# Kernel optimization log

Hardware: AMD Instinct MI355X
Metric: run time of the kernel (lower is better)

The kernel has to match this reference:

```python
import jax, jax.numpy as jnp
import numpy as np

B, NP, K = 8, 512, 64   # graphs, points per graph, knn neighbors
N = B * NP              # total nodes
EPS = 1e-5


def knn_edges(pos):
    """knn_graph(pos, k=K, batch, loop=True): edges (src=j neighbor, dst=i)."""
    p = pos.reshape(B, NP, 3)
    d2 = jnp.sum((p[:, :, None, :] - p[:, None, :, :]) ** 2, axis=-1)  # [B,NP,NP]
    _, idx = jax.lax.top_k(-d2, K)  # [B,NP,K] nearest (self included, d2=0)
    off = (jnp.arange(B, dtype=jnp.int32) * NP)[:, None, None]
    src = (idx.astype(jnp.int32) + off).reshape(-1)
    dst = jnp.broadcast_to(jnp.arange(NP, dtype=jnp.int32)[None, :, None] + off,
                           (B, NP, K)).reshape(-1)
    return src, dst


def graph_norm(x, batch, w, b, ms):
    """PyG GraphNorm: per-graph mean/std with learnable mean scale."""
    cnt = jax.ops.segment_sum(jnp.ones((x.shape[0], 1), x.dtype), batch, B)
    mean = jax.ops.segment_sum(x, batch, B) / cnt
    out = x - mean[batch] * ms
    var = jax.ops.segment_sum(out * out, batch, B) / cnt
    return w * out / jnp.sqrt(var + EPS)[batch] + b


def pointnet_layer(h, pos, src, dst, w1, b1, w2, b2):
    """message = MLP(concat(h_j, pos_j - pos_i)); aggregate = scatter-max over dst."""
    m = jnp.concatenate([h[src], pos[src] - pos[dst]], axis=-1)  # [E, Cin+3]
    m = jax.nn.relu(m @ w1 + b1) @ w2 + b2                        # [E, Cout]
    return jax.ops.segment_max(m, dst, N)


def _forward(batch, pos,
             gn1_w, gn1_b, gn1_ms, gn2_w, gn2_b, gn2_ms, gn3_w, gn3_b, gn3_ms,
             gn4_w, gn4_b, gn4_ms, gn5_w, gn5_b, gn5_ms, gn6_w, gn6_b, gn6_ms,
             c1_w1, c1_b1, c1_w2, c1_b2, c2_w1, c2_b1, c2_w2, c2_b2,
             c3_w1, c3_b1, c3_w2, c3_b2, c4_w1, c4_b1, c4_w2, c4_b2,
             c5_w1, c5_b1, c5_w2, c5_b2, cls_w, cls_b):
    src, dst = knn_edges(pos)
    h = graph_norm(pos, batch, gn1_w, gn1_b, gn1_ms)
    h = pointnet_layer(h, pos, src, dst, c1_w1, c1_b1, c1_w2, c1_b2)
    h = jax.nn.relu(graph_norm(h, batch, gn2_w, gn2_b, gn2_ms))
    h = pointnet_layer(h, pos, src, dst, c2_w1, c2_b1, c2_w2, c2_b2)
    h = jax.nn.relu(graph_norm(h, batch, gn3_w, gn3_b, gn3_ms))
    h = pointnet_layer(h, pos, src, dst, c3_w1, c3_b1, c3_w2, c3_b2)
    h = jax.nn.relu(graph_norm(h, batch, gn4_w, gn4_b, gn4_ms))
    h = pointnet_layer(h, pos, src, dst, c4_w1, c4_b1, c4_w2, c4_b2)
    h = jax.nn.relu(graph_norm(h, batch, gn5_w, gn5_b, gn5_ms))
    h = pointnet_layer(h, pos, src, dst, c5_w1, c5_b1, c5_w2, c5_b2)
    h = jax.nn.relu(graph_norm(h, batch, gn6_w, gn6_b, gn6_ms))
    return h @ cls_w + cls_b  # [N, 14]


def setup_inputs() -> dict:
    key = jax.random.key(0)
    ks = iter(jax.random.split(key, 40))
    inp = {}
    inp["pos"] = jax.random.normal(next(ks), (N, 3), jnp.float32)
    inp["batch"] = jnp.repeat(jnp.arange(B, dtype=jnp.int32), NP)
    for i, c in enumerate([3, 64, 128, 256, 512, 512], 1):
        inp[f"gn{i}_w"] = jnp.ones((c,), jnp.float32)
        inp[f"gn{i}_b"] = jnp.zeros((c,), jnp.float32)
        inp[f"gn{i}_ms"] = jnp.ones((c,), jnp.float32)
    for i, (ci, co) in enumerate([(3, 64), (64, 128), (128, 256), (256, 512), (512, 512)], 1):
        fin = ci + 3
        inp[f"c{i}_w1"] = jax.random.normal(next(ks), (fin, co), jnp.float32) / np.sqrt(fin).astype(np.float32)
        inp[f"c{i}_b1"] = jnp.zeros((co,), jnp.float32)
        inp[f"c{i}_w2"] = jax.random.normal(next(ks), (co, co), jnp.float32) / np.sqrt(co).astype(np.float32)
        inp[f"c{i}_b2"] = jnp.zeros((co,), jnp.float32)
    inp["cls_w"] = jax.random.normal(next(ks), (512, 14), jnp.float32) / np.float32(np.sqrt(512))
    inp["cls_b"] = jnp.zeros((14,), jnp.float32)
    return inp


def reference(pos, batch,
              gn1_w, gn1_b, gn1_ms, gn2_w, gn2_b, gn2_ms, gn3_w, gn3_b, gn3_ms,
              gn4_w, gn4_b, gn4_ms, gn5_w, gn5_b, gn5_ms, gn6_w, gn6_b, gn6_ms,
              c1_w1, c1_b1, c1_w2, c1_b2, c2_w1, c2_b1, c2_w2, c2_b2,
              c3_w1, c3_b1, c3_w2, c3_b2, c4_w1, c4_b1, c4_w2, c4_b2,
              c5_w1, c5_b1, c5_w2, c5_b2, cls_w, cls_b):
    return _forward(batch, pos,
                    gn1_w, gn1_b, gn1_ms, gn2_w, gn2_b, gn2_ms, gn3_w, gn3_b, gn3_ms,
                    gn4_w, gn4_b, gn4_ms, gn5_w, gn5_b, gn5_ms, gn6_w, gn6_b, gn6_ms,
                    c1_w1, c1_b1, c1_w2, c1_b2, c2_w1, c2_b1, c2_w2, c2_b2,
                    c3_w1, c3_b1, c3_w2, c3_b2, c4_w1, c4_b1, c4_w2, c4_b2,
                    c5_w1, c5_b1, c5_w2, c5_b2, cls_w, cls_b)
```

## Files before the change

kernel.cpp:

```cpp
#include <hip/hip_runtime.h>
#include <stdint.h>

#define N_NODES 4096
#define NGRAPH 8
#define NPTS 512
#define KNN 64
#define EPSN 1e-5f

typedef _Float16 f16x8 __attribute__((ext_vector_type(8)));
typedef float f32x4 __attribute__((ext_vector_type(4)));
typedef unsigned long long u64;

__device__ __forceinline__ unsigned short f2h(float f) {
    _Float16 h = (_Float16)f;
    union { _Float16 h; unsigned short u; } cv; cv.h = h;
    return cv.u;
}

__device__ __forceinline__ void w2cv(const float* __restrict__ src, unsigned short* __restrict__ dst,
                                     int off, int lg2c) {
    int C = 1 << lg2c;
    int k = off >> lg2c, n = off & (C - 1);
    int d = ((n >> 4) * (C / 32) + (k >> 5)) * 512 + ((k >> 3) & 3) * 128 + (n & 15) * 8 + (k & 7);
    dst[d] = f2h(src[off]);
}

__global__ __launch_bounds__(64) void setup_kernel(const float* __restrict__ pos, int* __restrict__ knn_out,
                                                   const float* __restrict__ wa, const float* __restrict__ wb,
                                                   const float* __restrict__ wc, const float* __restrict__ wd,
                                                   const float* __restrict__ we,
                                                   unsigned short* __restrict__ oa, unsigned short* __restrict__ ob,
                                                   unsigned short* __restrict__ oc, unsigned short* __restrict__ od,
                                                   unsigned short* __restrict__ oe,
                                                   float* __restrict__ statz,
                                                   const float* __restrict__ ms1, const float* __restrict__ gw1,
                                                   float* __restrict__ Aa, float* __restrict__ Sa) {
#pragma clang fp contract(off)
    __shared__ float px[NPTS], py[NPTS], pz[NPTS];
    __shared__ u64 keys[NPTS];
    int bid = blockIdx.x;
    int tid = threadIdx.x;
    int gidx = bid * 64 + tid;
    for (int idx = gidx; idx < 40960; idx += 262144) statz[idx] = 0.f;
    for (int idx = gidx; idx < 610304; idx += 262144) {
        if (idx < 4096)        w2cv(wa, oa, idx, 6);
        else if (idx < 20480)  w2cv(wb, ob, idx - 4096, 7);
        else if (idx < 86016)  w2cv(wc, oc, idx - 20480, 8);
        else if (idx < 348160) w2cv(wd, od, idx - 86016, 9);
        else                   w2cv(we, oe, idx - 348160, 9);
    }
    if (bid < 24) {
        int g = bid / 3, ch = bid - g * 3;
        float s1 = 0.f, s2 = 0.f;
        for (int n = tid; n < NPTS; n += 64) {
            float v = pos[(g * NPTS + n) * 3 + ch];
            s1 += v; s2 += v * v;
        }
        #pragma unroll
        for (int off = 32; off; off >>= 1) { s1 += __shfl_xor(s1, off); s2 += __shfl_xor(s2, off); }
        if (tid == 0) {
            float mean = s1 * (1.f / NPTS);
            float av = mean * ms1[ch];
            float var = s2 * (1.f / NPTS) - 2.f * av * mean + av * av;
            Aa[g * 3 + ch] = av;
            Sa[g * 3 + ch] = gw1[ch] / sqrtf(var + EPSN);
        }
    }
    int b = bid >> 9;
    int il = bid & (NPTS - 1);
    for (int n = tid; n < NPTS; n += 64) {
        int base = (b * NPTS + n) * 3;
        px[n] = pos[base]; py[n] = pos[base + 1]; pz[n] = pos[base + 2];
    }
    __syncthreads();
    float xi = px[il], yi = py[il], zi = pz[il];
    for (int n = tid; n < NPTS; n += 64) {
        float dx = px[n] - xi, dy = py[n] - yi, dz = pz[n] - zi;
        float d2 = dx * dx;
        d2 = d2 + dy * dy;
        d2 = d2 + dz * dz;
        keys[n] = (((u64)__float_as_uint(d2)) << 32) | (unsigned)n;
    }
    __syncthreads();
    for (int k2 = 2; k2 <= NPTS; k2 <<= 1) {
        for (int j = k2 >> 1; j > 0; j >>= 1) {
            #pragma unroll 4
            for (int p = 0; p < 4; ++p) {
                int pid = tid + p * 64;
                int t = ((pid & ~(j - 1)) << 1) | (pid & (j - 1));
                int ixj = t | j;
                u64 a = keys[t], c = keys[ixj];
                bool up = ((t & k2) == 0);
                if ((a > c) == up) { keys[t] = c; keys[ixj] = a; }
            }
            __syncthreads();
        }
    }
    int j0 = (int)(keys[tid] & 0xffffffffu);
    knn_out[(size_t)(b * NPTS + il) * KNN + tid] = b * NPTS + j0;
}

template<int CIN, int C, int RELU, int RAW>
__global__ __launch_bounds__(C) void node_kernel(const float* __restrict__ y, const float* __restrict__ pos,
                                                 const float* __restrict__ p1, const float* __restrict__ p2,
                                                 const float* __restrict__ ms, const float* __restrict__ gw,
                                                 const float* __restrict__ bnp,
                                                 const float* __restrict__ w1, const float* __restrict__ b1,
                                                 float* __restrict__ U, float* __restrict__ P) {
    constexpr int ROWS = 16;
    constexpr int KC = 64;
    constexpr int LDH = KC + 4;
    __shared__ float hs[ROWS][LDH];
    __shared__ float As_[CIN > 0 ? CIN : 1], Ss_[CIN > 0 ? CIN : 1];
    const int c = threadIdx.x;
    const int n0 = blockIdx.x * ROWS;
    const int b = n0 >> 9;
    if (RAW) {
        for (int ch = c; ch < CIN; ch += C) {
            float s1 = p1[b * CIN + ch], s2 = p2[b * CIN + ch];
            float mean = s1 * (1.f / NPTS);
            float a = mean * ms[ch];
            float var = s2 * (1.f / NPTS) - 2.f * a * mean + a * a;
            As_[ch] = a;
            Ss_[ch] = gw[ch] / sqrtf(var + EPSN);
        }
    }
    float acc[ROWS];
    #pragma unroll
    for (int r = 0; r < ROWS; ++r) acc[r] = 0.f;
    constexpr int NCHUNK = (CIN + KC - 1) / KC;
    #pragma unroll 1
    for (int s = 0; s < NCHUNK; ++s) {
        const int k0 = s * KC;
        const int kc = (CIN - k0 < KC) ? (CIN - k0) : KC;
        __syncthreads();
        for (int idx = c; idx < ROWS * kc; idx += C) {
            int r = idx / kc, k = idx - r * kc;
            int ch = k0 + k;
            float a = RAW ? As_[ch] : p1[b * CIN + ch];
            float sf = RAW ? Ss_[ch] : p2[b * CIN + ch];
            float v = (y[(size_t)(n0 + r) * CIN + ch] - a) * sf + bnp[ch];
            if (RELU) v = fmaxf(v, 0.f);
            hs[r][k] = v;
        }
        __syncthreads();
        int k = 0;
        for (; k + 4 <= kc; k += 4) {
            float w0 = w1[(size_t)(k0 + k) * C + c];
            float w1v = w1[(size_t)(k0 + k + 1) * C + c];
            float w2v = w1[(size_t)(k0 + k + 2) * C + c];
            float w3v = w1[(size_t)(k0 + k + 3) * C + c];
            #pragma unroll
            for (int r = 0; r < ROWS; ++r) {
                f32x4 hv = *(const f32x4*)&hs[r][k];
                acc[r] = fmaf(hv[0], w0, acc[r]);
                acc[r] = fmaf(hv[1], w1v, acc[r]);
                acc[r] = fmaf(hv[2], w2v, acc[r]);
                acc[r] = fmaf(hv[3], w3v, acc[r]);
            }
        }
        for (; k < kc; ++k) {
            float wv = w1[(size_t)(k0 + k) * C + c];
            #pragma unroll
            for (int r = 0; r < ROWS; ++r)
                acc[r] = fmaf(hs[r][k], wv, acc[r]);
        }
    }
    float pacc[ROWS];
    #pragma unroll
    for (int r = 0; r < ROWS; ++r) pacc[r] = 0.f;
    #pragma unroll
    for (int e = 0; e < 3; ++e) {
        float wv = w1[(size_t)(CIN + e) * C + c];
        #pragma unroll
        for (int r = 0; r < ROWS; ++r)
            pacc[r] = fmaf(pos[(n0 + r) * 3 + e], wv, pacc[r]);
    }
    float bv = b1[c];
    #pragma unroll
    for (int r = 0; r < ROWS; ++r) {
        U[(size_t)(n0 + r) * C + c] = acc[r] + pacc[r] + bv;
        P[(size_t)(n0 + r) * C + c] = pacc[r];
    }
}

template<int C, int W>
__global__ __launch_bounds__(W * 64, 4) void edge_kernel(const float* __restrict__ U, const float* __restrict__ P,
                                                         const int* __restrict__ knn, const unsigned short* __restrict__ w2t,
                                                         const float* __restrict__ b2, float* __restrict__ Y,
                                                         float* __restrict__ sum1, float* __restrict__ sum2) {
    constexpr int NCT = C / (W * 16);
    constexpr int S32 = C / 32;
    constexpr int NCHUNK = C / 8;
    __shared__ unsigned short Th[64 * C];
    __shared__ int jn[64];
    __shared__ float Pr[C];
    const int bid = blockIdx.x;
    const int i = ((bid & 7) << 9) | (bid >> 3);
    const int tid = threadIdx.x;
    const int wave = tid >> 6, lane = tid & 63, m = lane & 15, quad = lane >> 4;
    const int cw = wave * (NCT * 16);
    if (tid < 64) jn[tid] = knn[(size_t)i * KNN + tid];
    for (int idx = tid; idx < C; idx += W * 64) Pr[idx] = P[(size_t)i * C + idx];
    __syncthreads();
    #pragma unroll 2
    for (int idx = tid; idx < 64 * NCHUNK; idx += W * 64) {
        int row = idx / NCHUNK, ch = idx - row * NCHUNK;
        const float* up = U + (size_t)jn[row] * C + ch * 8;
        f32x4 va = *(const f32x4*)up;
        f32x4 vb = *(const f32x4*)(up + 4);
        f32x4 pa = *(const f32x4*)&Pr[ch * 8];
        f32x4 pb = *(const f32x4*)&Pr[ch * 8 + 4];
        uint4 pk;
        pk.x = (unsigned)f2h(fmaxf(va[0] - pa[0], 0.f)) | ((unsigned)f2h(fmaxf(va[1] - pa[1], 0.f)) << 16);
        pk.y = (unsigned)f2h(fmaxf(va[2] - pa[2], 0.f)) | ((unsigned)f2h(fmaxf(va[3] - pa[3], 0.f)) << 16);
        pk.z = (unsigned)f2h(fmaxf(vb[0] - pb[0], 0.f)) | ((unsigned)f2h(fmaxf(vb[1] - pb[1], 0.f)) << 16);
        pk.w = (unsigned)f2h(fmaxf(vb[2] - pb[2], 0.f)) | ((unsigned)f2h(fmaxf(vb[3] - pb[3], 0.f)) << 16);
        int sc = (ch & ~7) | ((ch ^ row) & 7);
        *(uint4*)&Th[row * C + sc * 8] = pk;
    }
    __syncthreads();
    f32x4 acc[4][NCT];
    f32x4 zero = {0.f, 0.f, 0.f, 0.f};
    #pragma unroll
    for (int rt = 0; rt < 4; ++rt)
        #pragma unroll
        for (int ct = 0; ct < NCT; ++ct)
            acc[rt][ct] = zero;
    #pragma unroll 2
    for (int s = 0; s < S32; ++s) {
        f16x8 a[4];
        #pragma unroll
        for (int rt = 0; rt < 4; ++rt) {
            int row = rt * 16 + m;
            int chunk = s * 4 + quad;
            int sc = (chunk & ~7) | ((chunk ^ row) & 7);
            a[rt] = *(const f16x8*)&Th[row * C + sc * 8];
        }
        #pragma unroll
        for (int ct = 0; ct < NCT; ++ct) {
            const f16x8 bb = *(const f16x8*)(w2t +
                (size_t)(((cw >> 4) + ct) * S32 + s) * 512 + quad * 128 + m * 8);
            #pragma unroll
            for (int rt = 0; rt < 4; ++rt)
                acc[rt][ct] = __builtin_amdgcn_mfma_f32_16x16x32_f16(a[rt], bb, acc[rt][ct], 0, 0, 0);
        }
    }
    const int gb = i >> 9;
    #pragma unroll
    for (int ct = 0; ct < NCT; ++ct) {
        float vmax = -3.4e38f;
        #pragma unroll
        for (int rt = 0; rt < 4; ++rt) {
            vmax = fmaxf(vmax, acc[rt][ct][0]);
            vmax = fmaxf(vmax, acc[rt][ct][1]);
            vmax = fmaxf(vmax, acc[rt][ct][2]);
            vmax = fmaxf(vmax, acc[rt][ct][3]);
        }
        vmax = fmaxf(vmax, __shfl_xor(vmax, 16));
        vmax = fmaxf(vmax, __shfl_xor(vmax, 32));
        if (quad == 0) {
            int col = cw + ct * 16 + m;
            float val = vmax + b2[col];
            Y[(size_t)i * C + col] = val;
            atomicAdd(&sum1[gb * C + col], val);
            atomicAdd(&sum2[gb * C + col], val * val);
        }
    }
}

__device__ __forceinline__ uint4 pack8(f32x4 va, f32x4 vb, f32x4 pa, f32x4 pb) {
    uint4 pk;
    pk.x = (unsigned)f2h(fmaxf(va[0] - pa[0], 0.f)) | ((unsigned)f2h(fmaxf(va[1] - pa[1], 0.f)) << 16);
    pk.y = (unsigned)f2h(fmaxf(va[2] - pa[2], 0.f)) | ((unsigned)f2h(fmaxf(va[3] - pa[3], 0.f)) << 16);
    pk.z = (unsigned)f2h(fmaxf(vb[0] - pb[0], 0.f)) | ((unsigned)f2h(fmaxf(vb[1] - pb[1], 0.f)) << 16);
    pk.w = (unsigned)f2h(fmaxf(vb[2] - pb[2], 0.f)) | ((unsigned)f2h(fmaxf(vb[3] - pb[3], 0.f)) << 16);
    return pk;
}

template<int C>
__global__ __launch_bounds__(512, 2) void edgeb_kernel(const float* __restrict__ U, const float* __restrict__ P,
                                                       const int* __restrict__ knn, const unsigned short* __restrict__ w2t,
                                                       const float* __restrict__ b2, float* __restrict__ Y,
                                                       float* __restrict__ sum1, float* __restrict__ sum2) {
    constexpr int NCT = C / 128;
    constexpr int S32 = C / 32;
    constexpr int NCHK = C / 8;
    constexpr int RSTEP = 512 / NCHK;
    __shared__ unsigned short Th[(C / 64) * 128 * 64];
    __shared__ int jn[128];
    const int bid = blockIdx.x;
    const int g = bid & 7;
    const int n0 = (g << 9) | ((bid >> 3) << 1);
    const int tid = threadIdx.x;
    const int lane = tid & 63, wave = tid >> 6, m = lane & 15, quad = lane >> 4;
    const int cw = wave * (NCT * 16);
    if (tid < 128) jn[tid] = knn[(size_t)(n0 + (tid >> 6)) * KNN + (tid & 63)];
    const int ch = tid & (NCHK - 1);
    const int rb = tid / NCHK;
    const int cblk = ch >> 3, cw8 = ch & 7;
    const float* pp = P + (size_t)n0 * C + ch * 8;
    f32x4 pa0 = *(const f32x4*)pp;
    f32x4 pb0 = *(const f32x4*)(pp + 4);
    f32x4 pa1 = *(const f32x4*)(pp + C);
    f32x4 pb1 = *(const f32x4*)(pp + C + 4);
    __syncthreads();
    #pragma unroll 4
    for (int t = 0; t < 128 / RSTEP; ++t) {
        int row = rb + t * RSTEP;
        const float* up = U + (size_t)jn[row] * C + ch * 8;
        f32x4 va = *(const f32x4*)up;
        f32x4 vb = *(const f32x4*)(up + 4);
        f32x4 pa = (row & 64) ? pa1 : pa0;
        f32x4 pb = (row & 64) ? pb1 : pb0;
        *(uint4*)&Th[cblk * 8192 + row * 64 + ((cw8 ^ (row & 7)) << 3)] = pack8(va, vb, pa, pb);
    }
    __syncthreads();
    f32x4 acc[8][NCT];
    f32x4 zero = {0.f, 0.f, 0.f, 0.f};
    #pragma unroll
    for (int rt = 0; rt < 8; ++rt)
        #pragma unroll
        for (int ct = 0; ct < NCT; ++ct)
            acc[rt][ct] = zero;
    const unsigned short* wt = w2t + (size_t)(cw >> 4) * S32 * 512 + quad * 128 + m * 8;
    f16x8 bbA[NCT], bbB[NCT], bbC[NCT], bbD[NCT];
    #pragma unroll
    for (int ct = 0; ct < NCT; ++ct) {
        bbA[ct] = *(const f16x8*)(wt + ((size_t)ct * S32 + 0) * 512);
        bbB[ct] = *(const f16x8*)(wt + ((size_t)ct * S32 + 1) * 512);
        bbC[ct] = *(const f16x8*)(wt + ((size_t)ct * S32 + 2) * 512);
        bbD[ct] = *(const f16x8*)(wt + ((size_t)ct * S32 + 3) * 512);
    }
    auto step = [&](f16x8 (&buf)[NCT], int scur, int snext, bool pre) {
        f16x8 a[8];
        int kc = scur * 4 + quad, cb = kc >> 3, wi = kc & 7;
        #pragma unroll
        for (int rt = 0; rt < 8; ++rt) {
            int row = rt * 16 + m;
            a[rt] = *(const f16x8*)&Th[cb * 8192 + row * 64 + ((wi ^ (row & 7)) << 3)];
        }
        #pragma unroll
        for (int ct = 0; ct < NCT; ++ct) {
            f16x8 bcur = buf[ct];
            if (pre) buf[ct] = *(const f16x8*)(wt + ((size_t)ct * S32 + snext) * 512);
            #pragma unroll
            for (int rt = 0; rt < 8; ++rt)
                acc[rt][ct] = __builtin_amdgcn_mfma_f32_16x16x32_f16(a[rt], bcur, acc[rt][ct], 0, 0, 0);
        }
    };
    #pragma unroll 1
    for (int s = 0; s + 4 < S32; s += 4) {
        step(bbA, s,     s + 4, true);
        step(bbB, s + 1, s + 5, true);
        step(bbC, s + 2, s + 6, true);
        step(bbD, s + 3, s + 7, true);
    }
    {
        int s = S32 - 4;
        step(bbA, s,     0, false);
        step(bbB, s + 1, 0, false);
        step(bbC, s + 2, 0, false);
        step(bbD, s + 3, 0, false);
    }
    #pragma unroll
    for (int h = 0; h < 2; ++h) {
        #pragma unroll
        for (int ct = 0; ct < NCT; ++ct) {
            float vmax = -3.4e38f;
            #pragma unroll
            for (int rt = h * 4; rt < h * 4 + 4; ++rt) {
                vmax = fmaxf(vmax, acc[rt][ct][0]);
                vmax = fmaxf(vmax, acc[rt][ct][1]);
                vmax = fmaxf(vmax, acc[rt][ct][2]);
                vmax = fmaxf(vmax, acc[rt][ct][3]);
            }
            vmax = fmaxf(vmax, __shfl_xor(vmax, 16));
            vmax = fmaxf(vmax, __shfl_xor(vmax, 32));
            if (quad == 0) {
                int col = cw + ct * 16 + m;
                float val = vmax + b2[col];
                Y[(size_t)(n0 + h) * C + col] = val;
                atomicAdd(&sum1[g * C + col], val);
                atomicAdd(&sum2[g * C + col], val * val);
            }
        }
    }
}

__global__ __launch_bounds__(256) void cls_kernel(const float* __restrict__ y, const float* __restrict__ sum1,
                                                  const float* __restrict__ sum2, const float* __restrict__ ms,
                                                  const float* __restrict__ gw, const float* __restrict__ gnb,
                                                  const float* __restrict__ w, const float* __restrict__ bias,
                                                  float* __restrict__ out) {
    __shared__ float wl[512 * 14];
    __shared__ _Float16 hn[16][520];
    __shared__ float As[512], Ss[512];
    int tid = threadIdx.x;
    int n0 = blockIdx.x * 16;
    int b = n0 >> 9;
    for (int ch = tid; ch < 512; ch += 256) {
        float s1 = sum1[b * 512 + ch], s2 = sum2[b * 512 + ch];
        float mean = s1 * (1.f / NPTS);
        float a = mean * ms[ch];
        float var = s2 * (1.f / NPTS) - 2.f * a * mean + a * a;
        As[ch] = a;
        Ss[ch] = gw[ch] / sqrtf(var + EPSN);
    }
    for (int idx = tid; idx < 512 * 14; idx += 256) wl[idx] = w[idx];
    __syncthreads();
    for (int idx = tid; idx < 16 * 512; idx += 256) {
        int r = idx >> 9, k = idx & 511;
        float v = (y[(size_t)(n0 + r) * 512 + k] - As[k]) * Ss[k] + gnb[k];
        hn[r][k] = (_Float16)fmaxf(v, 0.f);
    }
    __syncthreads();
    if (tid < 224) {
        int nl = tid / 14, c = tid - nl * 14;
        float acc = bias[c];
        for (int k = 0; k < 512; ++k)
            acc += (float)hn[nl][k] * wl[k * 14 + c];
        out[(size_t)(n0 + nl) * 14 + c] = acc;
    }
}

extern "C" void kernel_launch(void* const* d_in, const int* in_sizes, int n_in,
                              void* d_out, int out_size, void* d_ws, size_t ws_size,
                              hipStream_t stream) {
    const float* pos = (const float*)d_in[0];
    const float* gnw[6]; const float* gnb[6]; const float* gnms[6];
    for (int i = 0; i < 6; ++i) {
        gnw[i]  = (const float*)d_in[2 + 3 * i];
        gnb[i]  = (const float*)d_in[3 + 3 * i];
        gnms[i] = (const float*)d_in[4 + 3 * i];
    }
    const float* cw1[5]; const float* cb1[5]; const float* cw2[5]; const float* cb2[5];
    for (int i = 0; i < 5; ++i) {
        cw1[i] = (const float*)d_in[20 + 4 * i];
        cb1[i] = (const float*)d_in[21 + 4 * i];
        cw2[i] = (const float*)d_in[22 + 4 * i];
        cb2[i] = (const float*)d_in[23 + 4 * i];
    }
    const float* clsw = (const float*)d_in[40];
    const float* clsb = (const float*)d_in[41];
    float* out = (float*)d_out;

    char* ws = (char*)d_ws;
    int* knn             = (int*)(ws + 0);
    float* U             = (float*)(ws + 1048576);
    float* P             = (float*)(ws + 9437184);
    float* y             = (float*)(ws + 26214400);
    float* Aa            = (float*)(ws + 34603008);
    float* Sa            = (float*)(ws + 34619392);
    unsigned short* w2t0 = (unsigned short*)(ws + 34635776);
    unsigned short* w2t1 = (unsigned short*)(ws + 34643968);
    unsigned short* w2t2 = (unsigned short*)(ws + 34676736);
    unsigned short* w2t3 = (unsigned short*)(ws + 34807808);
    unsigned short* w2t4 = (unsigned short*)(ws + 35332096);
    float* acc           = (float*)(ws + 35856384);
    float* s1l[5]; float* s2l[5];
    for (int l = 0; l < 5; ++l) { s1l[l] = acc + l * 8192; s2l[l] = s1l[l] + 4096; }

    setup_kernel<<<N_NODES, 64, 0, stream>>>(pos, knn, cw2[0], cw2[1], cw2[2], cw2[3], cw2[4],
                                             w2t0, w2t1, w2t2, w2t3, w2t4, acc,
                                             gnms[0], gnw[0], Aa, Sa);

    node_kernel<3, 64, 0, 0><<<N_NODES / 16, 64, 0, stream>>>(pos, pos, Aa, Sa, gnms[0], gnw[0], gnb[0], cw1[0], cb1[0], U, P);
    edge_kernel<64, 4><<<N_NODES, 256, 0, stream>>>(U, P, knn, w2t0, cb2[0], y, s1l[0], s2l[0]);

    node_kernel<64, 128, 1, 1><<<N_NODES / 16, 128, 0, stream>>>(y, pos, s1l[0], s2l[0], gnms[1], gnw[1], gnb[1], cw1[1], cb1[1], U, P);
    edge_kernel<128, 8><<<N_NODES, 512, 0, stream>>>(U, P, knn, w2t1, cb2[1], y, s1l[1], s2l[1]);

    node_kernel<128, 256, 1, 1><<<N_NODES / 16, 256, 0, stream>>>(y, pos, s1l[1], s2l[1], gnms[2], gnw[2], gnb[2], cw1[2], cb1[2], U, P);
    edgeb_kernel<256><<<N_NODES / 2, 512, 0, stream>>>(U, P, knn, w2t2, cb2[2], y, s1l[2], s2l[2]);

    node_kernel<256, 512, 1, 1><<<N_NODES / 16, 512, 0, stream>>>(y, pos, s1l[2], s2l[2], gnms[3], gnw[3], gnb[3], cw1[3], cb1[3], U, P);
    edgeb_kernel<512><<<N_NODES / 2, 512, 0, stream>>>(U, P, knn, w2t3, cb2[3], y, s1l[3], s2l[3]);

    node_kernel<512, 512, 1, 1><<<N_NODES / 16, 512, 0, stream>>>(y, pos, s1l[3], s2l[3], gnms[4], gnw[4], gnb[4], cw1[4], cb1[4], U, P);
    edgeb_kernel<512><<<N_NODES / 2, 512, 0, stream>>>(U, P, knn, w2t4, cb2[4], y, s1l[4], s2l[4]);

    cls_kernel<<<N_NODES / 16, 256, 0, stream>>>(y, s1l[4], s2l[4], gnms[5], gnw[5], gnb[5], clsw, clsb, out);
}
```

Before: 719.7 us.

## Switch edge GEMM to 32x32x16 MFMA with new weight and LDS swizzle layouts

The edge-level second MLP GEMM now uses 32x32x16 f16 MFMA instead of 16x16x32, with four 32-row tiles and 32-column tiles per wave. The weight repacking for layers 3-5 and the LDS swizzle change to match the new operand layout, and setprio brackets the MFMA bursts. The aim is fewer MFMA issues and fewer LDS A-fragment loads per FLOP. The max reduction changes to match the new accumulator layout, and larger accumulators raise register pressure, which could lower occupancy.

```diff
diff --git a/kernel.cpp b/kernel.cpp
--- a/kernel.cpp
+++ b/kernel.cpp
@@ -9,6 +9,7 @@
 
 typedef _Float16 f16x8 __attribute__((ext_vector_type(8)));
 typedef float f32x4 __attribute__((ext_vector_type(4)));
+typedef float f32x16 __attribute__((ext_vector_type(16)));
 typedef unsigned long long u64;
 
 __device__ __forceinline__ unsigned short f2h(float f) {
@@ -22,6 +23,14 @@
     int C = 1 << lg2c;
     int k = off >> lg2c, n = off & (C - 1);
     int d = ((n >> 4) * (C / 32) + (k >> 5)) * 512 + ((k >> 3) & 3) * 128 + (n & 15) * 8 + (k & 7);
+    dst[d] = f2h(src[off]);
+}
+
+__device__ __forceinline__ void w2cv32(const float* __restrict__ src, unsigned short* __restrict__ dst,
+                                       int off, int lg2c) {
+    int C = 1 << lg2c;
+    int k = off >> lg2c, n = off & (C - 1);
+    int d = ((n >> 5) * (C / 16) + (k >> 4)) * 512 + (n & 31) * 8 + (((k >> 3) & 1) << 8) + (k & 7);
     dst[d] = f2h(src[off]);
 }
 
@@ -45,9 +54,9 @@
     for (int idx = gidx; idx < 610304; idx += 262144) {
         if (idx < 4096)        w2cv(wa, oa, idx, 6);
         else if (idx < 20480)  w2cv(wb, ob, idx - 4096, 7);
-        else if (idx < 86016)  w2cv(wc, oc, idx - 20480, 8);
-        else if (idx < 348160) w2cv(wd, od, idx - 86016, 9);
-        else                   w2cv(we, oe, idx - 348160, 9);
+        else if (idx < 86016)  w2cv32(wc, oc, idx - 20480, 8);
+        else if (idx < 348160) w2cv32(wd, od, idx - 86016, 9);
+        else                   w2cv32(we, oe, idx - 348160, 9);
     }
     if (bid < 24) {
         int g = bid / 3, ch = bid - g * 3;
@@ -283,8 +292,8 @@
                                                        const int* __restrict__ knn, const unsigned short* __restrict__ w2t,
                                                        const float* __restrict__ b2, float* __restrict__ Y,
                                                        float* __restrict__ sum1, float* __restrict__ sum2) {
-    constexpr int NCT = C / 128;
-    constexpr int S32 = C / 32;
+    constexpr int NCT = C / 256;
+    constexpr int S16 = C / 16;
     constexpr int NCHK = C / 8;
     constexpr int RSTEP = 512 / NCHK;
     __shared__ unsigned short Th[(C / 64) * 128 * 64];
@@ -293,12 +302,11 @@
     const int g = bid & 7;
     const int n0 = (g << 9) | ((bid >> 3) << 1);
     const int tid = threadIdx.x;
-    const int lane = tid & 63, wave = tid >> 6, m = lane & 15, quad = lane >> 4;
-    const int cw = wave * (NCT * 16);
+    const int lane = tid & 63, wave = tid >> 6;
+    const int l31 = lane & 31, lh = lane >> 5;
     if (tid < 128) jn[tid] = knn[(size_t)(n0 + (tid >> 6)) * KNN + (tid & 63)];
     const int ch = tid & (NCHK - 1);
     const int rb = tid / NCHK;
-    const int cblk = ch >> 3, cw8 = ch & 7;
     const float* pp = P + (size_t)n0 * C + ch * 8;
     f32x4 pa0 = *(const f32x4*)pp;
     f32x4 pb0 = *(const f32x4*)(pp + 4);
@@ -313,51 +321,54 @@
         f32x4 vb = *(const f32x4*)(up + 4);
         f32x4 pa = (row & 64) ? pa1 : pa0;
         f32x4 pb = (row & 64) ? pb1 : pb0;
-        *(uint4*)&Th[cblk * 8192 + row * 64 + ((cw8 ^ (row & 7)) << 3)] = pack8(va, vb, pa, pb);
-    }
-    __syncthreads();
-    f32x4 acc[8][NCT];
-    f32x4 zero = {0.f, 0.f, 0.f, 0.f};
-    #pragma unroll
-    for (int rt = 0; rt < 8; ++rt)
+        int ph = (ch & ~15) | ((ch ^ row) & 15);
+        *(uint4*)&Th[(ph >> 3) * 8192 + row * 64 + ((ph & 7) << 3)] = pack8(va, vb, pa, pb);
+    }
+    __syncthreads();
+    f32x16 acc[4][NCT];
+    #pragma unroll
+    for (int rt = 0; rt < 4; ++rt)
         #pragma unroll
         for (int ct = 0; ct < NCT; ++ct)
-            acc[rt][ct] = zero;
-    const unsigned short* wt = w2t + (size_t)(cw >> 4) * S32 * 512 + quad * 128 + m * 8;
+            acc[rt][ct] = (f32x16)0.f;
+    const unsigned short* wt = w2t + (size_t)(wave * NCT) * S16 * 512 + l31 * 8 + lh * 256;
     f16x8 bbA[NCT], bbB[NCT], bbC[NCT], bbD[NCT];
     #pragma unroll
     for (int ct = 0; ct < NCT; ++ct) {
-        bbA[ct] = *(const f16x8*)(wt + ((size_t)ct * S32 + 0) * 512);
-        bbB[ct] = *(const f16x8*)(wt + ((size_t)ct * S32 + 1) * 512);
-        bbC[ct] = *(const f16x8*)(wt + ((size_t)ct * S32 + 2) * 512);
-        bbD[ct] = *(const f16x8*)(wt + ((size_t)ct * S32 + 3) * 512);
+        bbA[ct] = *(const f16x8*)(wt + ((size_t)ct * S16 + 0) * 512);
+        bbB[ct] = *(const f16x8*)(wt + ((size_t)ct * S16 + 1) * 512);
+        bbC[ct] = *(const f16x8*)(wt + ((size_t)ct * S16 + 2) * 512);
+        bbD[ct] = *(const f16x8*)(wt + ((size_t)ct * S16 + 3) * 512);
     }
     auto step = [&](f16x8 (&buf)[NCT], int scur, int snext, bool pre) {
-        f16x8 a[8];
-        int kc = scur * 4 + quad, cb = kc >> 3, wi = kc & 7;
-        #pragma unroll
-        for (int rt = 0; rt < 8; ++rt) {
-            int row = rt * 16 + m;
-            a[rt] = *(const f16x8*)&Th[cb * 8192 + row * 64 + ((wi ^ (row & 7)) << 3)];
+        f16x8 a[4];
+        int kc8 = scur * 2 + lh;
+        #pragma unroll
+        for (int rt = 0; rt < 4; ++rt) {
+            int row = rt * 32 + l31;
+            int ph = (kc8 & ~15) | ((kc8 ^ row) & 15);
+            a[rt] = *(const f16x8*)&Th[(ph >> 3) * 8192 + row * 64 + ((ph & 7) << 3)];
         }
         #pragma unroll
         for (int ct = 0; ct < NCT; ++ct) {
             f16x8 bcur = buf[ct];
-            if (pre) buf[ct] = *(const f16x8*)(wt + ((size_t)ct * S32 + snext) * 512);
+            if (pre) buf[ct] = *(const f16x8*)(wt + ((size_t)ct * S16 + snext) * 512);
+            __builtin_amdgcn_s_setprio(1);
             #pragma unroll
-            for (int rt = 0; rt < 8; ++rt)
-                acc[rt][ct] = __builtin_amdgcn_mfma_f32_16x16x32_f16(a[rt], bcur, acc[rt][ct], 0, 0, 0);
+            for (int rt = 0; rt < 4; ++rt)
+                acc[rt][ct] = __builtin_amdgcn_mfma_f32_32x32x16_f16(a[rt], bcur, acc[rt][ct], 0, 0, 0);
+            __builtin_amdgcn_s_setprio(0);
         }
     };
     #pragma unroll 1
-    for (int s = 0; s + 4 < S32; s += 4) {
+    for (int s = 0; s + 4 < S16; s += 4) {
         step(bbA, s,     s + 4, true);
         step(bbB, s + 1, s + 5, true);
         step(bbC, s + 2, s + 6, true);
         step(bbD, s + 3, s + 7, true);
     }
     {
-        int s = S32 - 4;
+        int s = S16 - 4;
         step(bbA, s,     0, false);
         step(bbB, s + 1, 0, false);
         step(bbC, s + 2, 0, false);
@@ -369,16 +380,13 @@
         for (int ct = 0; ct < NCT; ++ct) {
             float vmax = -3.4e38f;
             #pragma unroll
-            for (int rt = h * 4; rt < h * 4 + 4; ++rt) {
-                vmax = fmaxf(vmax, acc[rt][ct][0]);
-                vmax = fmaxf(vmax, acc[rt][ct][1]);
-                vmax = fmaxf(vmax, acc[rt][ct][2]);
-                vmax = fmaxf(vmax, acc[rt][ct][3]);
-            }
-            vmax = fmaxf(vmax, __shfl_xor(vmax, 16));
+            for (int rt = 2 * h; rt < 2 * h + 2; ++rt)
+                #pragma unroll
+                for (int r = 0; r < 16; ++r)
+                    vmax = fmaxf(vmax, acc[rt][ct][r]);
             vmax = fmaxf(vmax, __shfl_xor(vmax, 32));
-            if (quad == 0) {
-                int col = cw + ct * 16 + m;
+            if (lh == 0) {
+                int col = wave * (NCT * 32) + ct * 32 + l31;
                 float val = vmax + b2[col];
                 Y[(size_t)(n0 + h) * C + col] = val;
                 atomicAdd(&sum1[g * C + col], val);
```

Result: slower. 747.6 us (+3.9%).
